# Kernel tuning notes

Measured on AMD Instinct MI355X. Metric: run time of the kernel, lower is better.

The kernel has to match this reference:

```python
import jax, jax.numpy as jnp
import numpy as np

B, N, H, K = 8192, 256, 2048, 1
BETA = 0.99
LOG2PI = float(np.log(2.0 * np.pi))


def V(z, Wv):
    # quadratic Lyapunov-style function; one positive value per sample (keepdims)
    u = z @ Wv
    return jnp.sum(u * u, axis=-1, keepdims=True) + 1e-3


def setup_inputs() -> dict:
    key = jax.random.key(0)
    ks = jax.random.split(key, 6)
    s1 = 1.0 / np.sqrt(N)
    s2 = 1.0 / np.sqrt(H)
    return {
        "x": jax.random.normal(ks[0], (B, N), jnp.float32),
        "y": jax.random.normal(ks[1], (B, 1, N), jnp.float32),
        "eps": jax.random.normal(ks[2], (B, 1, N), jnp.float32),
        "W1": jax.random.normal(ks[3], (N, H), jnp.float32) * s1,
        "b1": jnp.zeros((H,), jnp.float32),
        "W2": jax.random.normal(ks[4], (H, 2 * N), jnp.float32) * s2,
        "b2": jnp.zeros((2 * N,), jnp.float32),
        "Wv": jax.random.normal(ks[5], (N, N), jnp.float32) * s1,
    }


def reference(x, y, eps, W1, b1, W2, b2, Wv):
    # fhat: 2-layer MLP -> [B, 2N] = concat(mu, logvar)
    h = jnp.tanh(x @ W1 + b1)
    f = h @ W2 + b2
    mu, logvar = jnp.split(f, 2, axis=-1)            # [B, K*N] each (K=1)
    # torch: stack(split(mu, N, dim=1)).view(-1, 1, N)
    mu = mu.reshape(B, K, N).transpose(1, 0, 2).reshape(B * K, 1, N)
    var = jnp.exp(logvar).reshape(B, K, N).transpose(1, 0, 2).reshape(B * K, 1, N)
    # Lyapunov rescaling of the mean (per-sample scalar scale)
    Vx = V(x, Wv)[:, None, :]                        # [B,1,1]
    Vmu = V(mu, Wv)                                  # [B,1,1]
    bVx = BETA * Vx
    mu_stable = mu * ((bVx - jax.nn.relu(bVx - Vmu)) / Vmu)
    # reparameterized sample of diagonal MVN
    fx = mu_stable + jnp.sqrt(var) * eps             # [B,1,N]
    # diagonal-MVN log_prob, single fused pass
    q = (y - mu_stable) ** 2 / var
    logp = -0.5 * (N * LOG2PI + jnp.sum(jnp.log(var) + q, axis=-1))  # [B,1]
    logp_y = -jnp.sum(logp)
    return fx, logp_y
```

## Files before the change

kernel.cpp:

```cpp
#include <hip/hip_runtime.h>
#include <stdint.h>

#define B_SZ 8192
#define N_SZ 256
#define H_SZ 2048
#define LOG2PI_F 1.8378770664093453f
#define BETA_F 0.99f

typedef unsigned short ushort_t;
typedef __attribute__((ext_vector_type(8))) __bf16 bf16x8;
typedef __attribute__((ext_vector_type(4))) float f32x4;
typedef __attribute__((ext_vector_type(8))) ushort_t u16x8;

__device__ __forceinline__ ushort_t f2bf(float f) {
    unsigned int u = __float_as_uint(f);
    unsigned int r = (u + 0x7FFFu + ((u >> 16) & 1u)) >> 16;
    return (ushort_t)r;
}

__device__ __forceinline__ float fast_tanh(float v) {
    float ex = __expf(2.0f * v);
    return 1.0f - __fdividef(2.0f, ex + 1.0f);
}

__device__ __forceinline__ void async_ld16(const void* g, const char* lds_uniform) {
    __builtin_amdgcn_global_load_lds(
        (const __attribute__((address_space(1))) void*)g,
        (__attribute__((address_space(3))) void*)lds_uniform,
        16, 0, 0);
}

__global__ __launch_bounds__(256, 4)
void gemm1_vx_kernel(const ushort_t* __restrict__ xb, const ushort_t* __restrict__ W1p,
                     const ushort_t* __restrict__ Wvp, const float* __restrict__ b1,
                     ushort_t* __restrict__ h, float* __restrict__ vxp)
{
    __shared__ __align__(16) char smem[32768];
    char* sA = smem;
    char* sB = smem + 16384;
    const int tid = threadIdx.x;
    const int lane = tid & 63;
    const int w = tid >> 6;
    const int q = lane >> 4;
    const int rlo = lane & 15;
    const int wr = w >> 1, wc = w & 1;

    const int bid = blockIdx.x;
    const int r8 = bid & 7;
    const int u = bid >> 3;
    const int cb = u % 18;
    const int tb = u / 18;
    const int row0 = (r8 + 8 * tb) * 128;

    const bool w1path = cb < 16;
    const int n0 = (w1path ? cb : cb - 16) * 128;
    const ushort_t* Bp = w1path ? W1p : Wvp;
    const int N = w1path ? H_SZ : N_SZ;

    f32x4 acc[4][4];
#pragma unroll
    for (int i = 0; i < 4; ++i)
#pragma unroll
        for (int j = 0; j < 4; ++j)
            acc[i][j] = f32x4{0.f, 0.f, 0.f, 0.f};

    for (int k0 = 0; k0 < N_SZ; k0 += 64) {
        __syncthreads();
#pragma unroll
        for (int r = 0; r < 4; ++r) {
            int c = r * 256 + tid;
            int kq = c >> 7, m = c & 127;
            async_ld16(xb + (size_t)(row0 + m) * N_SZ + k0 + kq * 8, sA + (c << 4));
        }
        int ko0 = k0 >> 3;
#pragma unroll
        for (int r = 0; r < 4; ++r) {
            int c = r * 256 + tid;
            int kq = c >> 7, n = c & 127;
            async_ld16(Bp + ((size_t)(ko0 + kq) * N + n0 + n) * 8, sB + (c << 4));
        }
        __syncthreads();

#pragma unroll
        for (int ks = 0; ks < 2; ++ks) {
            int kq = ks * 4 + q;
            bf16x8 af[4], bfr[4];
#pragma unroll
            for (int i = 0; i < 4; ++i)
                af[i] = *(const bf16x8*)(sA + (((kq << 7) + wr * 64 + i * 16 + rlo) << 4));
#pragma unroll
            for (int j = 0; j < 4; ++j)
                bfr[j] = *(const bf16x8*)(sB + (((kq << 7) + wc * 64 + j * 16 + rlo) << 4));
#pragma unroll
            for (int i = 0; i < 4; ++i)
#pragma unroll
                for (int j = 0; j < 4; ++j)
                    acc[i][j] = __builtin_amdgcn_mfma_f32_16x16x32_bf16(af[i], bfr[j], acc[i][j], 0, 0, 0);
        }
    }

    if (w1path) {
#pragma unroll
        for (int j = 0; j < 4; ++j) {
            int col = n0 + wc * 64 + j * 16 + rlo;
            float bv = b1[col];
#pragma unroll
            for (int i = 0; i < 4; ++i) {
                int rowb = row0 + wr * 64 + i * 16 + q * 4;
#pragma unroll
                for (int rr = 0; rr < 4; ++rr)
                    h[(size_t)(rowb + rr) * H_SZ + col] = f2bf(fast_tanh(acc[i][j][rr] + bv));
            }
        }
    } else {
        float* vdst = vxp + (n0 >> 7) * B_SZ;
#pragma unroll
        for (int i = 0; i < 4; ++i) {
#pragma unroll
            for (int rr = 0; rr < 4; ++rr) {
                float s = 0.f;
#pragma unroll
                for (int j = 0; j < 4; ++j) { float v = acc[i][j][rr]; s += v * v; }
#pragma unroll
                for (int m = 1; m < 16; m <<= 1) s += __shfl_xor(s, m, 64);
                if (rlo == 0)
                    vdst[row0 + wr * 64 + i * 16 + q * 4 + rr] = s;
            }
        }
    }
}

__global__ __launch_bounds__(256, 2)
void gemm2_kernel(const ushort_t* __restrict__ h, const ushort_t* __restrict__ W2p,
                  const float* __restrict__ b2, float* __restrict__ f,
                  ushort_t* __restrict__ mub)
{
    __shared__ __align__(16) char smem[49152];
    char* sA = smem;
    char* sB = smem + 16384;
    const int tid = threadIdx.x;
    const int lane = tid & 63;
    const int w = tid >> 6;
    const int q = lane >> 4;
    const int rlo = lane & 15;
    const int wr = w >> 1, wc = w & 1;

    const int bid = blockIdx.x;
    const int r8 = bid & 7;
    const int u = bid >> 3;
    const int cb = u & 3;
    const int tb = u >> 2;
    const int row0 = (r8 + 8 * tb) * 64;
    const int n0 = cb * 128;

    f32x4 acc[2][4];
#pragma unroll
    for (int i = 0; i < 2; ++i)
#pragma unroll
        for (int j = 0; j < 4; ++j)
            acc[i][j] = f32x4{0.f, 0.f, 0.f, 0.f};

    for (int k0 = 0; k0 < H_SZ; k0 += 128) {
        __syncthreads();
#pragma unroll
        for (int r = 0; r < 4; ++r) {
            int c = r * 256 + tid;
            int kq = c >> 6, m = c & 63;
            async_ld16(h + (size_t)(row0 + m) * H_SZ + k0 + kq * 8, sA + (c << 4));
        }
        int ko0 = k0 >> 3;
#pragma unroll
        for (int r = 0; r < 8; ++r) {
            int c = r * 256 + tid;
            int kq = c >> 7, n = c & 127;
            async_ld16(W2p + ((size_t)(ko0 + kq) * 512 + n0 + n) * 8, sB + (c << 4));
        }
        __syncthreads();

#pragma unroll
        for (int ks = 0; ks < 4; ++ks) {
            int kq = ks * 4 + q;
            bf16x8 af[2], bfr[4];
#pragma unroll
            for (int i = 0; i < 2; ++i)
                af[i] = *(const bf16x8*)(sA + (((kq << 6) + wr * 32 + i * 16 + rlo) << 4));
#pragma unroll
            for (int j = 0; j < 4; ++j)
                bfr[j] = *(const bf16x8*)(sB + (((kq << 7) + wc * 64 + j * 16 + rlo) << 4));
#pragma unroll
            for (int i = 0; i < 2; ++i)
#pragma unroll
                for (int j = 0; j < 4; ++j)
                    acc[i][j] = __builtin_amdgcn_mfma_f32_16x16x32_bf16(af[i], bfr[j], acc[i][j], 0, 0, 0);
        }
    }

#pragma unroll
    for (int j = 0; j < 4; ++j) {
        int col = n0 + wc * 64 + j * 16 + rlo;
        float bv = b2[col];
#pragma unroll
        for (int i = 0; i < 2; ++i) {
            int rowb = row0 + wr * 32 + i * 16 + q * 4;
#pragma unroll
            for (int rr = 0; rr < 4; ++rr) {
                float v = acc[i][j][rr] + bv;
                f[(size_t)(rowb + rr) * 512 + col] = v;
                if (col < N_SZ)
                    mub[(size_t)(rowb + rr) * N_SZ + col] = f2bf(v);
            }
        }
    }
}

__global__ __launch_bounds__(256)
void vmu_epilogue_kernel(const ushort_t* __restrict__ mub, const ushort_t* __restrict__ Wvp,
                         const float* __restrict__ f, const float* __restrict__ y,
                         const float* __restrict__ eps, const float* __restrict__ vxp,
                         float* __restrict__ out, float* __restrict__ partials)
{
    __shared__ float vsum[4][16];
    __shared__ float vmu_s[16];
    __shared__ float red[4];
    const int tid = threadIdx.x;
    const int lane = tid & 63;
    const int w = tid >> 6;
    const int q = lane >> 4;
    const int rlo = lane & 15;
    const int r0 = blockIdx.x * 16;

    f32x4 acc[4];
#pragma unroll
    for (int j = 0; j < 4; ++j)
        acc[j] = f32x4{0.f, 0.f, 0.f, 0.f};

    const ushort_t* a0 = mub + (size_t)(r0 + rlo) * N_SZ + q * 8;
    const ushort_t* b0 = Wvp + ((size_t)q * N_SZ + w * 64 + rlo) * 8;
#pragma unroll
    for (int s = 0; s < 8; ++s) {
        bf16x8 af = *(const bf16x8*)(a0 + s * 32);
        bf16x8 bfr[4];
#pragma unroll
        for (int j = 0; j < 4; ++j)
            bfr[j] = *(const bf16x8*)(b0 + s * 4 * N_SZ * 8 + j * 128);
#pragma unroll
        for (int j = 0; j < 4; ++j)
            acc[j] = __builtin_amdgcn_mfma_f32_16x16x32_bf16(af, bfr[j], acc[j], 0, 0, 0);
    }
#pragma unroll
    for (int rr = 0; rr < 4; ++rr) {
        float s = 0.f;
#pragma unroll
        for (int j = 0; j < 4; ++j) { float v = acc[j][rr]; s += v * v; }
#pragma unroll
        for (int m = 1; m < 16; m <<= 1) s += __shfl_xor(s, m, 64);
        if (rlo == 0) vsum[w][q * 4 + rr] = s;
    }
    __syncthreads();
    if (tid < 16)
        vmu_s[tid] = 1e-3f + vsum[0][tid] + vsum[1][tid] + vsum[2][tid] + vsum[3][tid];
    __syncthreads();

    float t = 0.f;
    const int n = tid;
#pragma unroll 4
    for (int r = 0; r < 16; ++r) {
        size_t row = (size_t)(r0 + r);
        float mu = f[row * 512 + n];
        float lv = f[row * 512 + 256 + n];
        float var = expf(lv);
        float Vx = vxp[row] + vxp[B_SZ + row] + 1e-3f;
        float Vmu = vmu_s[r];
        float scale = fminf(BETA_F * Vx, Vmu) / Vmu;
        float mus = mu * scale;
        out[row * 256 + n] = mus + sqrtf(var) * eps[row * 256 + n];
        float d = y[row * 256 + n] - mus;
        t += lv + d * d / var;
    }
#pragma unroll
    for (int m = 32; m >= 1; m >>= 1) t += __shfl_down(t, m, 64);
    if (lane == 0) red[w] = t;
    __syncthreads();
    if (tid == 0)
        partials[blockIdx.x] = red[0] + red[1] + red[2] + red[3];
}

__global__ __launch_bounds__(256)
void reduce_kernel(const float* __restrict__ partials, float* __restrict__ out)
{
    int tid = threadIdx.x;
    float s = partials[tid] + partials[tid + 256];
#pragma unroll
    for (int m = 32; m >= 1; m >>= 1) s += __shfl_down(s, m, 64);
    __shared__ float red[4];
    if ((tid & 63) == 0) red[tid >> 6] = s;
    __syncthreads();
    if (tid == 0)
        out[(size_t)B_SZ * N_SZ] =
            0.5f * (red[0] + red[1] + red[2] + red[3] +
                    (float)N_SZ * LOG2PI_F * (float)B_SZ);
}

__global__ __launch_bounds__(256)
void convert_kernel(const float* __restrict__ x, const float* __restrict__ W1,
                    const float* __restrict__ W2, const float* __restrict__ Wv,
                    ushort_t* __restrict__ xb, ushort_t* __restrict__ W1p,
                    ushort_t* __restrict__ W2p, ushort_t* __restrict__ Wvp)
{
    const int XC = 262144, W1C = 65536, W2C = 131072;
    int c = blockIdx.x * 256 + threadIdx.x;
    if (c < XC) {
        f32x4 a = *(const f32x4*)(x + (size_t)c * 8);
        f32x4 b = *(const f32x4*)(x + (size_t)c * 8 + 4);
        u16x8 o;
#pragma unroll
        for (int i = 0; i < 4; ++i) { o[i] = f2bf(a[i]); o[4 + i] = f2bf(b[i]); }
        *(u16x8*)(xb + (size_t)c * 8) = o;
    } else if (c < XC + W1C) {
        int d = c - XC;
        int ko = d >> 11, n = d & 2047;
        u16x8 o;
#pragma unroll
        for (int ki = 0; ki < 8; ++ki)
            o[ki] = f2bf(W1[(size_t)(ko * 8 + ki) * H_SZ + n]);
        *(u16x8*)(W1p + (size_t)d * 8) = o;
    } else if (c < XC + W1C + W2C) {
        int d = c - XC - W1C;
        int ko = d >> 9, n = d & 511;
        u16x8 o;
#pragma unroll
        for (int ki = 0; ki < 8; ++ki)
            o[ki] = f2bf(W2[(size_t)(ko * 8 + ki) * 512 + n]);
        *(u16x8*)(W2p + (size_t)d * 8) = o;
    } else {
        int d = c - XC - W1C - W2C;
        int ko = d >> 8, n = d & 255;
        u16x8 o;
#pragma unroll
        for (int ki = 0; ki < 8; ++ki)
            o[ki] = f2bf(Wv[(size_t)(ko * 8 + ki) * N_SZ + n]);
        *(u16x8*)(Wvp + (size_t)d * 8) = o;
    }
}

extern "C" void kernel_launch(void* const* d_in, const int* in_sizes, int n_in,
                              void* d_out, int out_size, void* d_ws, size_t ws_size,
                              hipStream_t stream)
{
    const float* x   = (const float*)d_in[0];
    const float* y   = (const float*)d_in[1];
    const float* eps = (const float*)d_in[2];
    const float* W1  = (const float*)d_in[3];
    const float* b1  = (const float*)d_in[4];
    const float* W2  = (const float*)d_in[5];
    const float* b2  = (const float*)d_in[6];
    const float* Wv  = (const float*)d_in[7];
    float* out = (float*)d_out;

    char* ws = (char*)d_ws;
    size_t off = 0;
    auto alloc = [&](size_t bytes) {
        char* p = ws + off;
        off += (bytes + 255) & ~(size_t)255;
        return p;
    };
    ushort_t* xb  = (ushort_t*)alloc((size_t)B_SZ * N_SZ * 2);
    ushort_t* W1p = (ushort_t*)alloc((size_t)N_SZ * H_SZ * 2);
    ushort_t* W2p = (ushort_t*)alloc((size_t)H_SZ * 512 * 2);
    ushort_t* Wvp = (ushort_t*)alloc((size_t)N_SZ * N_SZ * 2);
    ushort_t* h   = (ushort_t*)alloc((size_t)B_SZ * H_SZ * 2);
    float*    f   = (float*)alloc((size_t)B_SZ * 512 * 4);
    ushort_t* mub = (ushort_t*)alloc((size_t)B_SZ * N_SZ * 2);
    float*    vxp = (float*)alloc((size_t)2 * B_SZ * 4);
    float*    partials = (float*)alloc(512 * 4);

    const int TOTALC = 262144 + 65536 + 131072 + 8192;
    convert_kernel<<<TOTALC / 256, 256, 0, stream>>>(x, W1, W2, Wv, xb, W1p, W2p, Wvp);

    gemm1_vx_kernel<<<1152, 256, 0, stream>>>(xb, W1p, Wvp, b1, h, vxp);
    gemm2_kernel<<<512, 256, 0, stream>>>(h, W2p, b2, f, mub);
    vmu_epilogue_kernel<<<512, 256, 0, stream>>>(mub, Wvp, f, y, eps, vxp, out, partials);
    reduce_kernel<<<1, 256, 0, stream>>>(partials, out);
}
```

Measured before the change: 160.3 us.

## Stage GEMM1 output through LDS and store h in packed k-major layout

The GEMM1 epilogue previously wrote h with scattered 2-byte stores. It now writes the tile into LDS and then emits 16-byte vector stores in a k-chunk-major packed layout. GEMM2's A-loads are changed to read this layout, so each async 16-byte load hits contiguous rows rather than strided rows. The cost is extra LDS (34816 bytes), two barriers per block, and a layout shared between both kernels.

```diff
diff --git a/kernel.cpp b/kernel.cpp
--- a/kernel.cpp
+++ b/kernel.cpp
@@ -33,9 +33,9 @@
 __global__ __launch_bounds__(256, 4)
 void gemm1_vx_kernel(const ushort_t* __restrict__ xb, const ushort_t* __restrict__ W1p,
                      const ushort_t* __restrict__ Wvp, const float* __restrict__ b1,
-                     ushort_t* __restrict__ h, float* __restrict__ vxp)
-{
-    __shared__ __align__(16) char smem[32768];
+                     ushort_t* __restrict__ hp, float* __restrict__ vxp)
+{
+    __shared__ __align__(16) char smem[34816];
     char* sA = smem;
     char* sB = smem + 16384;
     const int tid = threadIdx.x;
@@ -100,17 +100,27 @@
     }
 
     if (w1path) {
+        __syncthreads();
+        ushort_t* st = (ushort_t*)smem;
 #pragma unroll
         for (int j = 0; j < 4; ++j) {
-            int col = n0 + wc * 64 + j * 16 + rlo;
-            float bv = b1[col];
+            int coll = wc * 64 + j * 16 + rlo;
+            float bv = b1[n0 + coll];
 #pragma unroll
             for (int i = 0; i < 4; ++i) {
-                int rowb = row0 + wr * 64 + i * 16 + q * 4;
+                int rowl = wr * 64 + i * 16 + q * 4;
 #pragma unroll
                 for (int rr = 0; rr < 4; ++rr)
-                    h[(size_t)(rowb + rr) * H_SZ + col] = f2bf(fast_tanh(acc[i][j][rr] + bv));
+                    st[(rowl + rr) * 136 + coll] = f2bf(fast_tanh(acc[i][j][rr] + bv));
             }
+        }
+        __syncthreads();
+#pragma unroll
+        for (int r = 0; r < 8; ++r) {
+            int c = r * 256 + tid;
+            int m = c & 127, ko = c >> 7;
+            u16x8 v = *(const u16x8*)(st + m * 136 + ko * 8);
+            *(u16x8*)(hp + ((size_t)((n0 >> 3) + ko) * B_SZ + row0 + m) * 8) = v;
         }
     } else {
         float* vdst = vxp + (n0 >> 7) * B_SZ;
@@ -131,7 +141,7 @@
 }
 
 __global__ __launch_bounds__(256, 2)
-void gemm2_kernel(const ushort_t* __restrict__ h, const ushort_t* __restrict__ W2p,
+void gemm2_kernel(const ushort_t* __restrict__ hp, const ushort_t* __restrict__ W2p,
                   const float* __restrict__ b2, float* __restrict__ f,
                   ushort_t* __restrict__ mub)
 {
@@ -162,13 +172,13 @@
 
     for (int k0 = 0; k0 < H_SZ; k0 += 128) {
         __syncthreads();
+        int ko0 = k0 >> 3;
 #pragma unroll
         for (int r = 0; r < 4; ++r) {
             int c = r * 256 + tid;
             int kq = c >> 6, m = c & 63;
-            async_ld16(h + (size_t)(row0 + m) * H_SZ + k0 + kq * 8, sA + (c << 4));
-        }
-        int ko0 = k0 >> 3;
+            async_ld16(hp + ((size_t)(ko0 + kq) * B_SZ + row0 + m) * 8, sA + (c << 4));
+        }
 #pragma unroll
         for (int r = 0; r < 8; ++r) {
             int c = r * 256 + tid;
@@ -368,7 +378,7 @@
     ushort_t* W1p = (ushort_t*)alloc((size_t)N_SZ * H_SZ * 2);
     ushort_t* W2p = (ushort_t*)alloc((size_t)H_SZ * 512 * 2);
     ushort_t* Wvp = (ushort_t*)alloc((size_t)N_SZ * N_SZ * 2);
-    ushort_t* h   = (ushort_t*)alloc((size_t)B_SZ * H_SZ * 2);
+    ushort_t* hp  = (ushort_t*)alloc((size_t)B_SZ * H_SZ * 2);
     float*    f   = (float*)alloc((size_t)B_SZ * 512 * 4);
     ushort_t* mub = (ushort_t*)alloc((size_t)B_SZ * N_SZ * 2);
     float*    vxp = (float*)alloc((size_t)2 * B_SZ * 4);
@@ -377,8 +387,8 @@
     const int TOTALC = 262144 + 65536 + 131072 + 8192;
     convert_kernel<<<TOTALC / 256, 256, 0, stream>>>(x, W1, W2, Wv, xb, W1p, W2p, Wvp);
 
-    gemm1_vx_kernel<<<1152, 256, 0, stream>>>(xb, W1p, Wvp, b1, h, vxp);
-    gemm2_kernel<<<512, 256, 0, stream>>>(h, W2p, b2, f, mub);
+    gemm1_vx_kernel<<<1152, 256, 0, stream>>>(xb, W1p, Wvp, b1, hp, vxp);
+    gemm2_kernel<<<512, 256, 0, stream>>>(hp, W2p, b2, f, mub);
     vmu_epilogue_kernel<<<512, 256, 0, stream>>>(mub, Wvp, f, y, eps, vxp, out, partials);
     reduce_kernel<<<1, 256, 0, stream>>>(partials, out);
 }
```

After: 155.4 us. 3.1% less time.
